# Optimization experiments

Hardware: AMD Instinct MI355X
Metric: run time of the kernel (lower is better)

The kernel has to match this reference:

```python
import jax, jax.numpy as jnp
import numpy as np

# Crossbar constants (from iterator / hard-coded in source)
V_REF = 0.25
G_MIN = 0.001
G_MAX = 0.005
N_AVG = 2.8
N_STD = 0.2

N_IN, N_OUT, BATCH = 1024, 512, 128


def setup_inputs() -> dict:
    key = jax.random.key(0)
    ks = jax.random.split(key, 6)
    stdv = 1.0 / np.sqrt(N_IN)
    x = jax.random.normal(ks[0], (BATCH, N_IN), jnp.float32)
    w_pos = 0.5 + stdv * jax.random.normal(ks[1], (N_IN, N_OUT), jnp.float32)
    w_neg = 0.5 + stdv * jax.random.normal(ks[2], (N_IN, N_OUT), jnp.float32)
    b_pos = jnp.full((N_OUT,), 0.5, jnp.float32)
    b_neg = jnp.full((N_OUT,), 0.5, jnp.float32)
    # per-device nonlinearity noise for the (n_in+1, 2*n_out) crossbar
    n_noise = jax.random.normal(ks[3], (N_IN + 1, 2 * N_OUT), jnp.float32)
    return {"x": x, "w_pos": w_pos, "w_neg": w_neg, "b_pos": b_pos,
            "b_neg": b_neg, "n_noise": n_noise}


def reference(x, w_pos, w_neg, b_pos, b_neg, n_noise):
    # --- assemble combined weights: biases appended as extra word line,
    # pos/neg columns interleaved -> (m, 2*n_out), m = n_in+1
    cw_pos = jnp.concatenate([w_pos, b_pos[None, :]], axis=0)
    cw_neg = jnp.concatenate([w_neg, b_neg[None, :]], axis=0)
    m = cw_pos.shape[0]
    weights = jnp.stack([cw_pos, cw_neg], axis=-1).reshape(m, -1)  # (m, 2*n_out)

    # --- map weight params to conductances: G = k_G * w + G_min
    max_weight = jnp.max(jnp.abs(weights))
    k_G = (G_MAX - G_MIN) / max_weight
    G = k_G * weights + G_MIN                      # (m, 2*n_out)

    # --- map inputs to voltages (extra column of ones for bias line)
    k_V = 2.0 * V_REF
    ones = jnp.ones((x.shape[0], 1), x.dtype)
    V = k_V * jnp.concatenate([x, ones], axis=1)   # (b, m)

    # --- nonlinear device currents: I = sign(V) * V_ref*G * (|V|/V_ref)^log2(n)
    n = N_AVG + N_STD * n_noise                    # (m, 2*n_out)
    exponent = jnp.log2(n)
    ratio = jnp.abs(V) / V_REF                     # (b, m)
    I_ind = (jnp.sign(V)[:, :, None]
             * (V_REF * G)[None, :, :]
             * ratio[:, :, None] ** exponent[None, :, :])  # (b, m, 2*n_out)

    # --- bit-line reduction, pos-neg differential, map current back to y
    I = jnp.sum(I_ind, axis=1)                     # (b, 2*n_out)
    I_total = I[:, 0::2] - I[:, 1::2]              # (b, n_out)
    y = I_total / (k_V * k_G)
    return y
```

## Files before the change

kernel.cpp:

```cpp
#include <hip/hip_runtime.h>

#define N_IN  1024
#define N_OUT 512
#define BATCH 128
#define M     (N_IN + 1)


#if defined(__has_builtin)
#  if __has_builtin(__builtin_amdgcn_exp2f)
#    define FAST_EXP2(x) __builtin_amdgcn_exp2f(x)
#  endif
#  if __has_builtin(__builtin_amdgcn_logf)
#    define FAST_LOG2(x) __builtin_amdgcn_logf(x)
#  endif
#endif
#ifndef FAST_EXP2
#  define FAST_EXP2(x) exp2f(x)
#endif
#ifndef FAST_LOG2
#  define FAST_LOG2(x) log2f(x)
#endif

__global__ __launch_bounds__(256)
void maxred_kernel(const float4* __restrict__ wp4, const float4* __restrict__ wn4,
                   const float* __restrict__ bp, const float* __restrict__ bn,
                   float* __restrict__ maxp, float* __restrict__ y)
{
    const int bid = blockIdx.x;
    const int t   = threadIdx.x;

    y[bid * 256 + t] = 0.0f;

    const int base = bid * 512;
    float m = 0.0f;
    #pragma unroll
    for (int r = 0; r < 2; ++r) {
        const float4 a = wp4[base + r * 256 + t];
        const float4 b = wn4[base + r * 256 + t];
        m = fmaxf(m, fmaxf(fmaxf(fabsf(a.x), fabsf(a.y)),
                           fmaxf(fabsf(a.z), fabsf(a.w))));
        m = fmaxf(m, fmaxf(fmaxf(fabsf(b.x), fabsf(b.y)),
                           fmaxf(fabsf(b.z), fabsf(b.w))));
    }
    if (bid == 0) {
        m = fmaxf(m, fmaxf(fabsf(bp[t]), fabsf(bp[t + 256])));
        m = fmaxf(m, fmaxf(fabsf(bn[t]), fabsf(bn[t + 256])));
    }
    #pragma unroll
    for (int off = 32; off > 0; off >>= 1)
        m = fmaxf(m, __shfl_xor(m, off, 64));

    __shared__ float wred[4];
    const int wid = t >> 6;
    if ((t & 63) == 0) wred[wid] = m;
    __syncthreads();
    if (t == 0)
        maxp[bid] = fmaxf(fmaxf(wred[0], wred[1]), fmaxf(wred[2], wred[3]));
}

#define CH 32
#define IC 32

__global__ __launch_bounds__(256, 4)
void memristor_main(const float* __restrict__ x,  const float* __restrict__ wp,
                    const float* __restrict__ wn, const float* __restrict__ bp,
                    const float* __restrict__ bn, const float* __restrict__ nn,
                    const float* __restrict__ maxp, float* __restrict__ y)
{
    __shared__ float4 lsq[CH][17];

    const int jlane = threadIdx.x & 63;
    const int bslot = __builtin_amdgcn_readfirstlane((int)(threadIdx.x >> 6));

    const int bid = blockIdx.x;
    const int jt  = bid & 7;
    const int bt  = (bid >> 3) & 3;
    const int ic  = bid >> 5;

    const int i0 = ic * CH;
    const int j  = jt * 64 + jlane;
    const int b0 = bt * 32;

    {
        const int ii = threadIdx.x & 31;
        const int b8 = threadIdx.x >> 5;
        #pragma unroll
        for (int r = 0; r < 4; ++r) {
            const int bb = b8 + r * 8;
            const float v = x[(b0 + bb) * N_IN + i0 + ii];
            const float s = (v > 0.0f) ? 1.0f : ((v < 0.0f) ? -1.0f : 0.0f);
            const float l = FAST_LOG2(2.0f * fabsf(v));
            reinterpret_cast<float2*>(&lsq[ii][0])[bb] = make_float2(l, s);
        }
    }

    float m = fmaxf(fmaxf(maxp[jlane], maxp[jlane + 64]),
                    fmaxf(maxp[jlane + 128], maxp[jlane + 192]));
    #pragma unroll
    for (int off = 32; off > 0; off >>= 1)
        m = fmaxf(m, __shfl_xor(m, off, 64));
    const float gofs = 0.125f * __uint_as_float(
        __builtin_amdgcn_readfirstlane(__float_as_uint(m)));

    __syncthreads();

    float acc[8];
    #pragma unroll
    for (int k = 0; k < 8; ++k) acc[k] = 0.0f;

    const float*  wprow = wp + (size_t)i0 * N_OUT + j;
    const float*  wnrow = wn + (size_t)i0 * N_OUT + j;
    const float2* nnrow = (const float2*)nn + (size_t)i0 * N_OUT + j;

    #pragma unroll 2
    for (int ii = 0; ii < CH; ++ii) {
        const float wpv  = wprow[ii * N_OUT];
        const float wnv  = wnrow[ii * N_OUT];
        const float2 np2 = nnrow[ii * N_OUT];
        const float ep  = FAST_LOG2(fmaf(0.2f, np2.x, 2.8f));
        const float en  = FAST_LOG2(fmaf(0.2f, np2.y, 2.8f));
        const float lgp = FAST_LOG2(fmaf(0.5f, wpv, gofs));
        const float lgn = FAST_LOG2(fmaf(0.5f, wnv, gofs));
        #pragma unroll
        for (int mm = 0; mm < 4; ++mm) {
            const float4 q = lsq[ii][bslot * 4 + mm];
            const float Ep0 = FAST_EXP2(fmaf(ep, q.x, lgp));
            const float En0 = FAST_EXP2(fmaf(en, q.x, lgn));
            acc[2 * mm]     = fmaf(q.y, Ep0 - En0, acc[2 * mm]);
            const float Ep1 = FAST_EXP2(fmaf(ep, q.z, lgp));
            const float En1 = FAST_EXP2(fmaf(en, q.z, lgn));
            acc[2 * mm + 1] = fmaf(q.w, Ep1 - En1, acc[2 * mm + 1]);
        }
    }

    if (ic == IC - 1) {
        const float2 np2 = ((const float2*)nn)[(size_t)N_IN * N_OUT + j];
        const float npp = fmaf(0.2f, np2.x, 2.8f);
        const float npn = fmaf(0.2f, np2.y, 2.8f);
        const float gp = fmaf(0.5f, bp[j], gofs);
        const float gn = fmaf(0.5f, bn[j], gofs);
        const float t  = fmaf(gp, npp, -(gn * npn));
        #pragma unroll
        for (int k = 0; k < 8; ++k) acc[k] += t;
    }

    #pragma unroll
    for (int k = 0; k < 8; ++k)
        atomicAdd(&y[(b0 + bslot * 8 + k) * N_OUT + j], acc[k]);
}

extern "C" void kernel_launch(void* const* d_in, const int* in_sizes, int n_in,
                              void* d_out, int out_size, void* d_ws, size_t ws_size,
                              hipStream_t stream)
{
    const float* x  = (const float*)d_in[0];
    const float* wp = (const float*)d_in[1];
    const float* wn = (const float*)d_in[2];
    const float* bp = (const float*)d_in[3];
    const float* bn = (const float*)d_in[4];
    const float* nn = (const float*)d_in[5];
    float* y        = (float*)d_out;
    float* maxp     = (float*)d_ws;

    maxred_kernel<<<256, 256, 0, stream>>>((const float4*)wp, (const float4*)wn,
                                           bp, bn, maxp, y);

    memristor_main<<<8 * 4 * IC, 256, 0, stream>>>(x, wp, wn, bp, bn, nn,
                                                   maxp, y);
}
```

Baseline: 92.24 us.

## Fuse max reduction into main kernel with cooperative grid barrier

```diff
diff --git a/kernel.cpp b/kernel.cpp
--- a/kernel.cpp
+++ b/kernel.cpp
@@ -5,6 +5,12 @@
 #define BATCH 128
 #define M     (N_IN + 1)
 
+#define WS_CNT_OFF  0
+#define WS_MAXP_OFF 256
+
+#define CH   32
+#define IC   32
+#define NBLK 1024
 
 #if defined(__has_builtin)
 #  if __has_builtin(__builtin_amdgcn_exp2f)
@@ -21,69 +27,32 @@
 #  define FAST_LOG2(x) log2f(x)
 #endif
 
-__global__ __launch_bounds__(256)
-void maxred_kernel(const float4* __restrict__ wp4, const float4* __restrict__ wn4,
-                   const float* __restrict__ bp, const float* __restrict__ bn,
-                   float* __restrict__ maxp, float* __restrict__ y)
-{
-    const int bid = blockIdx.x;
-    const int t   = threadIdx.x;
-
-    y[bid * 256 + t] = 0.0f;
-
-    const int base = bid * 512;
-    float m = 0.0f;
-    #pragma unroll
-    for (int r = 0; r < 2; ++r) {
-        const float4 a = wp4[base + r * 256 + t];
-        const float4 b = wn4[base + r * 256 + t];
-        m = fmaxf(m, fmaxf(fmaxf(fabsf(a.x), fabsf(a.y)),
-                           fmaxf(fabsf(a.z), fabsf(a.w))));
-        m = fmaxf(m, fmaxf(fmaxf(fabsf(b.x), fabsf(b.y)),
-                           fmaxf(fabsf(b.z), fabsf(b.w))));
-    }
-    if (bid == 0) {
-        m = fmaxf(m, fmaxf(fabsf(bp[t]), fabsf(bp[t + 256])));
-        m = fmaxf(m, fmaxf(fabsf(bn[t]), fabsf(bn[t + 256])));
-    }
-    #pragma unroll
-    for (int off = 32; off > 0; off >>= 1)
-        m = fmaxf(m, __shfl_xor(m, off, 64));
-
-    __shared__ float wred[4];
-    const int wid = t >> 6;
-    if ((t & 63) == 0) wred[wid] = m;
-    __syncthreads();
-    if (t == 0)
-        maxp[bid] = fmaxf(fmaxf(wred[0], wred[1]), fmaxf(wred[2], wred[3]));
-}
-
-#define CH 32
-#define IC 32
-
 __global__ __launch_bounds__(256, 4)
-void memristor_main(const float* __restrict__ x,  const float* __restrict__ wp,
-                    const float* __restrict__ wn, const float* __restrict__ bp,
-                    const float* __restrict__ bn, const float* __restrict__ nn,
-                    const float* __restrict__ maxp, float* __restrict__ y)
+void memristor_fused(const float* __restrict__ x,  const float* __restrict__ wp,
+                     const float* __restrict__ wn, const float* __restrict__ bp,
+                     const float* __restrict__ bn, const float* __restrict__ nn,
+                     unsigned* __restrict__ cnt,   float* __restrict__ maxp,
+                     float* __restrict__ y)
 {
     __shared__ float4 lsq[CH][17];
-
-    const int jlane = threadIdx.x & 63;
-    const int bslot = __builtin_amdgcn_readfirstlane((int)(threadIdx.x >> 6));
-
-    const int bid = blockIdx.x;
-    const int jt  = bid & 7;
-    const int bt  = (bid >> 3) & 3;
-    const int ic  = bid >> 5;
+    __shared__ float  wred[4];
+
+    const int tid   = threadIdx.x;
+    const int jlane = tid & 63;
+    const int bid   = blockIdx.x;
+    const int jt    = bid & 7;
+    const int bt    = (bid >> 3) & 3;
+    const int ic    = bid >> 5;
 
     const int i0 = ic * CH;
     const int j  = jt * 64 + jlane;
     const int b0 = bt * 32;
 
+    if (tid < 64) y[bid * 64 + tid] = 0.0f;
+
     {
-        const int ii = threadIdx.x & 31;
-        const int b8 = threadIdx.x >> 5;
+        const int ii = tid & 31;
+        const int b8 = tid >> 5;
         #pragma unroll
         for (int r = 0; r < 4; ++r) {
             const int bb = b8 + r * 8;
@@ -94,22 +63,47 @@
         }
     }
 
-    float m = fmaxf(fmaxf(maxp[jlane], maxp[jlane + 64]),
-                    fmaxf(maxp[jlane + 128], maxp[jlane + 192]));
+    const float* wprow = wp + (size_t)i0 * N_OUT + j;
+    const float* wnrow = wn + (size_t)i0 * N_OUT + j;
+    float m = 0.0f;
+    #pragma unroll 8
+    for (int ii = 0; ii < CH; ++ii)
+        m = fmaxf(m, fmaxf(fabsf(wprow[ii * N_OUT]), fabsf(wnrow[ii * N_OUT])));
+    if (ic == IC - 1)
+        m = fmaxf(m, fmaxf(fabsf(bp[j]), fabsf(bn[j])));
     #pragma unroll
     for (int off = 32; off > 0; off >>= 1)
         m = fmaxf(m, __shfl_xor(m, off, 64));
+    if ((tid & 63) == 0) wred[tid >> 6] = m;
+    __syncthreads();
+    if (tid == 0) {
+        const float bm = fmaxf(fmaxf(wred[0], wred[1]), fmaxf(wred[2], wred[3]));
+        atomicExch(&maxp[bid], bm);
+        __threadfence();
+        atomicAdd(cnt, 1u);
+        while (__hip_atomic_load(cnt, __ATOMIC_RELAXED,
+                                 __HIP_MEMORY_SCOPE_AGENT) < NBLK)
+            __builtin_amdgcn_s_sleep(1);
+    }
+    __syncthreads();
+
+    float gm = 0.0f;
+    #pragma unroll
+    for (int r = 0; r < 16; ++r)
+        gm = fmaxf(gm, __hip_atomic_load(&maxp[jlane + r * 64], __ATOMIC_RELAXED,
+                                         __HIP_MEMORY_SCOPE_AGENT));
+    #pragma unroll
+    for (int off = 32; off > 0; off >>= 1)
+        gm = fmaxf(gm, __shfl_xor(gm, off, 64));
     const float gofs = 0.125f * __uint_as_float(
-        __builtin_amdgcn_readfirstlane(__float_as_uint(m)));
-
-    __syncthreads();
+        __builtin_amdgcn_readfirstlane(__float_as_uint(gm)));
+
+    const int bslot = __builtin_amdgcn_readfirstlane(tid >> 6);
 
     float acc[8];
     #pragma unroll
     for (int k = 0; k < 8; ++k) acc[k] = 0.0f;
 
-    const float*  wprow = wp + (size_t)i0 * N_OUT + j;
-    const float*  wnrow = wn + (size_t)i0 * N_OUT + j;
     const float2* nnrow = (const float2*)nn + (size_t)i0 * N_OUT + j;
 
     #pragma unroll 2
@@ -149,6 +143,117 @@
         atomicAdd(&y[(b0 + bslot * 8 + k) * N_OUT + j], acc[k]);
 }
 
+__global__ __launch_bounds__(256)
+void maxred_kernel(const float4* __restrict__ wp4, const float4* __restrict__ wn4,
+                   const float* __restrict__ bp, const float* __restrict__ bn,
+                   float* __restrict__ maxp, float* __restrict__ y)
+{
+    const int bid = blockIdx.x;
+    const int t   = threadIdx.x;
+    y[bid * 256 + t] = 0.0f;
+    const int base = bid * 512;
+    float m = 0.0f;
+    #pragma unroll
+    for (int r = 0; r < 2; ++r) {
+        const float4 a = wp4[base + r * 256 + t];
+        const float4 b = wn4[base + r * 256 + t];
+        m = fmaxf(m, fmaxf(fmaxf(fabsf(a.x), fabsf(a.y)),
+                           fmaxf(fabsf(a.z), fabsf(a.w))));
+        m = fmaxf(m, fmaxf(fmaxf(fabsf(b.x), fabsf(b.y)),
+                           fmaxf(fabsf(b.z), fabsf(b.w))));
+    }
+    if (bid == 0) {
+        m = fmaxf(m, fmaxf(fabsf(bp[t]), fabsf(bp[t + 256])));
+        m = fmaxf(m, fmaxf(fabsf(bn[t]), fabsf(bn[t + 256])));
+    }
+    #pragma unroll
+    for (int off = 32; off > 0; off >>= 1)
+        m = fmaxf(m, __shfl_xor(m, off, 64));
+    __shared__ float wred[4];
+    const int wid = t >> 6;
+    if ((t & 63) == 0) wred[wid] = m;
+    __syncthreads();
+    if (t == 0)
+        maxp[bid] = fmaxf(fmaxf(wred[0], wred[1]), fmaxf(wred[2], wred[3]));
+}
+
+__global__ __launch_bounds__(256, 4)
+void memristor_main(const float* __restrict__ x,  const float* __restrict__ wp,
+                    const float* __restrict__ wn, const float* __restrict__ bp,
+                    const float* __restrict__ bn, const float* __restrict__ nn,
+                    const float* __restrict__ maxp, float* __restrict__ y)
+{
+    __shared__ float4 lsq[CH][17];
+    const int jlane = threadIdx.x & 63;
+    const int bslot = __builtin_amdgcn_readfirstlane((int)(threadIdx.x >> 6));
+    const int bid = blockIdx.x;
+    const int jt  = bid & 7;
+    const int bt  = (bid >> 3) & 3;
+    const int ic  = bid >> 5;
+    const int i0 = ic * CH;
+    const int j  = jt * 64 + jlane;
+    const int b0 = bt * 32;
+    {
+        const int ii = threadIdx.x & 31;
+        const int b8 = threadIdx.x >> 5;
+        #pragma unroll
+        for (int r = 0; r < 4; ++r) {
+            const int bb = b8 + r * 8;
+            const float v = x[(b0 + bb) * N_IN + i0 + ii];
+            const float s = (v > 0.0f) ? 1.0f : ((v < 0.0f) ? -1.0f : 0.0f);
+            const float l = FAST_LOG2(2.0f * fabsf(v));
+            reinterpret_cast<float2*>(&lsq[ii][0])[bb] = make_float2(l, s);
+        }
+    }
+    float m = fmaxf(fmaxf(maxp[jlane], maxp[jlane + 64]),
+                    fmaxf(maxp[jlane + 128], maxp[jlane + 192]));
+    #pragma unroll
+    for (int off = 32; off > 0; off >>= 1)
+        m = fmaxf(m, __shfl_xor(m, off, 64));
+    const float gofs = 0.125f * __uint_as_float(
+        __builtin_amdgcn_readfirstlane(__float_as_uint(m)));
+    __syncthreads();
+    float acc[8];
+    #pragma unroll
+    for (int k = 0; k < 8; ++k) acc[k] = 0.0f;
+    const float*  wprow = wp + (size_t)i0 * N_OUT + j;
+    const float*  wnrow = wn + (size_t)i0 * N_OUT + j;
+    const float2* nnrow = (const float2*)nn + (size_t)i0 * N_OUT + j;
+    #pragma unroll 2
+    for (int ii = 0; ii < CH; ++ii) {
+        const float wpv  = wprow[ii * N_OUT];
+        const float wnv  = wnrow[ii * N_OUT];
+        const float2 np2 = nnrow[ii * N_OUT];
+        const float ep  = FAST_LOG2(fmaf(0.2f, np2.x, 2.8f));
+        const float en  = FAST_LOG2(fmaf(0.2f, np2.y, 2.8f));
+        const float lgp = FAST_LOG2(fmaf(0.5f, wpv, gofs));
+        const float lgn = FAST_LOG2(fmaf(0.5f, wnv, gofs));
+        #pragma unroll
+        for (int mm = 0; mm < 4; ++mm) {
+            const float4 q = lsq[ii][bslot * 4 + mm];
+            const float Ep0 = FAST_EXP2(fmaf(ep, q.x, lgp));
+            const float En0 = FAST_EXP2(fmaf(en, q.x, lgn));
+            acc[2 * mm]     = fmaf(q.y, Ep0 - En0, acc[2 * mm]);
+            const float Ep1 = FAST_EXP2(fmaf(ep, q.z, lgp));
+            const float En1 = FAST_EXP2(fmaf(en, q.z, lgn));
+            acc[2 * mm + 1] = fmaf(q.w, Ep1 - En1, acc[2 * mm + 1]);
+        }
+    }
+    if (ic == IC - 1) {
+        const float2 np2 = ((const float2*)nn)[(size_t)N_IN * N_OUT + j];
+        const float npp = fmaf(0.2f, np2.x, 2.8f);
+        const float npn = fmaf(0.2f, np2.y, 2.8f);
+        const float gp = fmaf(0.5f, bp[j], gofs);
+        const float gn = fmaf(0.5f, bn[j], gofs);
+        const float t  = fmaf(gp, npp, -(gn * npn));
+        #pragma unroll
+        for (int k = 0; k < 8; ++k) acc[k] += t;
+    }
+    #pragma unroll
+    for (int k = 0; k < 8; ++k)
+        atomicAdd(&y[(b0 + bslot * 8 + k) * N_OUT + j], acc[k]);
+}
+
 extern "C" void kernel_launch(void* const* d_in, const int* in_sizes, int n_in,
                               void* d_out, int out_size, void* d_ws, size_t ws_size,
                               hipStream_t stream)
@@ -159,12 +264,22 @@
     const float* bp = (const float*)d_in[3];
     const float* bn = (const float*)d_in[4];
     const float* nn = (const float*)d_in[5];
-    float* y        = (float*)d_out;
-    float* maxp     = (float*)d_ws;
-
-    maxred_kernel<<<256, 256, 0, stream>>>((const float4*)wp, (const float4*)wn,
-                                           bp, bn, maxp, y);
-
-    memristor_main<<<8 * 4 * IC, 256, 0, stream>>>(x, wp, wn, bp, bn, nn,
-                                                   maxp, y);
-}
+    float*    y    = (float*)d_out;
+    unsigned* cnt  = (unsigned*)((char*)d_ws + WS_CNT_OFF);
+    float*    maxp = (float*)((char*)d_ws + WS_MAXP_OFF);
+
+    (void)hipMemsetAsync(cnt, 0, sizeof(unsigned), stream);
+
+    void* args[] = {(void*)&x, (void*)&wp, (void*)&wn, (void*)&bp, (void*)&bn,
+                    (void*)&nn, (void*)&cnt, (void*)&maxp, (void*)&y};
+    hipError_t err = hipLaunchCooperativeKernel(
+        (const void*)memristor_fused, dim3(NBLK), dim3(256), args, 0, stream);
+
+    if (err != hipSuccess) {
+        maxred_kernel<<<256, 256, 0, stream>>>((const float4*)wp,
+                                               (const float4*)wn, bp, bn,
+                                               maxp, y);
+        memristor_main<<<NBLK, 256, 0, stream>>>(x, wp, wn, bp, bn, nn,
+                                                 maxp, y);
+    }
+}
```

Result: slower. 202.1 us (+119.1%).
